# Performance work log

Measured on AMD Instinct MI355X. Metric: run time of the kernel, lower is better.

## Reference

```python
import jax, jax.numpy as jnp
import numpy as np

VOCAB = 32000
EMBED_DIM = 64
HIDDEN_NUM = 16
PAD_ID = 0
B, S = 128, 4096


def setup_inputs() -> dict:
    key = jax.random.key(0)
    k1, k2, k3, k4, k5, k6, k7 = jax.random.split(key, 7)
    # values serve as token ids (when mask==1) or numeric values (mask==0)
    input_ids = jax.random.randint(k1, (B, S), 0, VOCAB).astype(jnp.float32)
    type_mask = jax.random.randint(k2, (B, S), 0, 2).astype(jnp.int32)
    emb_table = jax.random.normal(k3, (VOCAB, EMBED_DIM), dtype=jnp.float32)
    emb_table = emb_table.at[PAD_ID].set(0.0)  # nn.Embedding padding_idx
    # numeric MLP: Linear(1,16) -> ReLU -> Linear(16,64)
    w1 = jax.random.normal(k4, (HIDDEN_NUM, 1), dtype=jnp.float32) * 0.5
    b1 = jax.random.normal(k5, (HIDDEN_NUM,), dtype=jnp.float32) * 0.1
    w2 = jax.random.normal(k6, (EMBED_DIM, HIDDEN_NUM), dtype=jnp.float32) * 0.25
    b2 = jax.random.normal(k7, (EMBED_DIM,), dtype=jnp.float32) * 0.1
    return {"input_ids": input_ids, "type_mask": type_mask,
            "emb_table": emb_table, "w1": w1, "b1": b1, "w2": w2, "b2": b2}


def reference(input_ids, type_mask, emb_table, w1, b1, w2, b2):
    # Faithful to Embedder.forward: token positions get embedding lookup,
    # numeric positions get a 2-layer MLP on the scalar value. Instead of
    # boolean gather/scatter (dynamic shapes), compute both paths densely
    # and select -- same math, jit-friendly, single pass.
    tok_mask = type_mask.astype(bool)                              # (B,S)
    ids = jnp.where(tok_mask, input_ids, 0).astype(jnp.int32)      # safe ids
    tok_emb = emb_table[ids]                                       # (B,S,D)
    x = input_ids[..., None]                                       # (B,S,1)
    h = jax.nn.relu(jnp.einsum('bsi,hi->bsh', x, w1) + b1)         # (B,S,16)
    num_emb = jnp.einsum('bsh,dh->bsd', h, w2) + b2                # (B,S,D)
    return jnp.where(tok_mask[..., None], tok_emb, num_emb)
```

## Files before the change

### kernel.cpp

```cpp
#include <hip/hip_runtime.h>

#define D 64
#define H 16

__global__ __launch_bounds__(256) void Embedder_kernel(
    const float* __restrict__ input_ids,
    const int*   __restrict__ type_mask,
    const float* __restrict__ emb,
    const float* __restrict__ w1,
    const float* __restrict__ b1,
    const float* __restrict__ w2,
    const float* __restrict__ b2,
    float*       __restrict__ out,
    int npos)
{
    __shared__ float s_w1[H];
    __shared__ float s_b1[H];
    __shared__ float s_b2[D];
    __shared__ float s_w2t[H * D];

    const int tid = threadIdx.x;
    if (tid < H) { s_w1[tid] = w1[tid]; s_b1[tid] = b1[tid]; }
    if (tid >= 64 && tid < 64 + D) s_b2[tid - 64] = b2[tid - 64];
    for (int i = tid; i < D * H; i += 256) {
        int d = i >> 4, j = i & 15;
        s_w2t[j * D + d] = w2[i];
    }
    __syncthreads();

    const int gid = blockIdx.x * 256 + tid;
    const int pos = gid >> 4;
    if (pos >= npos) return;
    const int d4 = (gid & 15) * 4;

    const float x = input_ids[pos];
    const int   m = type_mask[pos];

    float4 r;
    if (m) {
        const int id = (int)x;
        r = *reinterpret_cast<const float4*>(&emb[(size_t)id * D + d4]);
    } else {
        float h[H];
        #pragma unroll
        for (int j = 0; j < H; ++j)
            h[j] = fmaxf(fmaf(x, s_w1[j], s_b1[j]), 0.0f);
        float4 acc = *reinterpret_cast<const float4*>(&s_b2[d4]);
        #pragma unroll
        for (int j = 0; j < H; ++j) {
            const float4 w = *reinterpret_cast<const float4*>(&s_w2t[j * D + d4]);
            acc.x = fmaf(h[j], w.x, acc.x);
            acc.y = fmaf(h[j], w.y, acc.y);
            acc.z = fmaf(h[j], w.z, acc.z);
            acc.w = fmaf(h[j], w.w, acc.w);
        }
        r = acc;
    }
    *reinterpret_cast<float4*>(&out[(size_t)pos * D + d4]) = r;
}

extern "C" void kernel_launch(void* const* d_in, const int* in_sizes, int n_in,
                              void* d_out, int out_size, void* d_ws, size_t ws_size,
                              hipStream_t stream) {
    const float* input_ids = (const float*)d_in[0];
    const int*   type_mask = (const int*)d_in[1];
    const float* emb       = (const float*)d_in[2];
    const float* w1        = (const float*)d_in[3];
    const float* b1        = (const float*)d_in[4];
    const float* w2        = (const float*)d_in[5];
    const float* b2        = (const float*)d_in[6];
    float*       out       = (float*)d_out;

    const int npos = in_sizes[0];
    const long long nthreads = (long long)npos * 16;
    const int blocks = (int)((nthreads + 255) / 256);

    Embedder_kernel<<<blocks, 256, 0, stream>>>(
        input_ids, type_mask, emb, w1, b1, w2, b2, out, npos);
}
```

Baseline: 202.2 us.

## Process multiple positions per thread with register-resident MLP weights and branchless select

```diff
diff --git a/kernel.cpp b/kernel.cpp
--- a/kernel.cpp
+++ b/kernel.cpp
@@ -2,8 +2,11 @@
 
 #define D 64
 #define H 16
+#define PPT 16
 
-__global__ __launch_bounds__(256) void Embedder_kernel(
+typedef float f32x4 __attribute__((ext_vector_type(4)));
+
+__global__ __launch_bounds__(256, 3) void Embedder_kernel(
     const float* __restrict__ input_ids,
     const int*   __restrict__ type_mask,
     const float* __restrict__ emb,
@@ -14,49 +17,71 @@
     float*       __restrict__ out,
     int npos)
 {
-    __shared__ float s_w1[H];
-    __shared__ float s_b1[H];
-    __shared__ float s_b2[D];
-    __shared__ float s_w2t[H * D];
+    const int tid = threadIdx.x;
+    const int gid = blockIdx.x * 256 + tid;
+    const int T   = (npos * 16) / PPT;
+    if (gid >= T) return;
 
-    const int tid = threadIdx.x;
-    if (tid < H) { s_w1[tid] = w1[tid]; s_b1[tid] = b1[tid]; }
-    if (tid >= 64 && tid < 64 + D) s_b2[tid - 64] = b2[tid - 64];
-    for (int i = tid; i < D * H; i += 256) {
-        int d = i >> 4, j = i & 15;
-        s_w2t[j * D + d] = w2[i];
-    }
-    __syncthreads();
-
-    const int gid = blockIdx.x * 256 + tid;
-    const int pos = gid >> 4;
-    if (pos >= npos) return;
     const int d4 = (gid & 15) * 4;
 
-    const float x = input_ids[pos];
-    const int   m = type_mask[pos];
+    float w2s[4][H];
+    #pragma unroll
+    for (int r = 0; r < 4; ++r) {
+        #pragma unroll
+        for (int c = 0; c < 4; ++c) {
+            const f32x4 t = *reinterpret_cast<const f32x4*>(&w2[(d4 + r) * H + 4 * c]);
+            w2s[r][4*c+0] = t.x; w2s[r][4*c+1] = t.y;
+            w2s[r][4*c+2] = t.z; w2s[r][4*c+3] = t.w;
+        }
+    }
+    float w1r[H], b1r[H];
+    #pragma unroll
+    for (int c = 0; c < 4; ++c) {
+        const f32x4 tw = *reinterpret_cast<const f32x4*>(&w1[4*c]);
+        const f32x4 tb = *reinterpret_cast<const f32x4*>(&b1[4*c]);
+        w1r[4*c+0] = tw.x; w1r[4*c+1] = tw.y; w1r[4*c+2] = tw.z; w1r[4*c+3] = tw.w;
+        b1r[4*c+0] = tb.x; b1r[4*c+1] = tb.y; b1r[4*c+2] = tb.z; b1r[4*c+3] = tb.w;
+    }
+    const f32x4 b2s = *reinterpret_cast<const f32x4*>(&b2[d4]);
 
-    float4 r;
-    if (m) {
-        const int id = (int)x;
-        r = *reinterpret_cast<const float4*>(&emb[(size_t)id * D + d4]);
-    } else {
-        float h[H];
-        #pragma unroll
-        for (int j = 0; j < H; ++j)
-            h[j] = fmaxf(fmaf(x, s_w1[j], s_b1[j]), 0.0f);
-        float4 acc = *reinterpret_cast<const float4*>(&s_b2[d4]);
+    const int pbase = gid >> 4;
+    const int pstep = T >> 4;
+
+    #pragma unroll 1
+    for (int k = 0; k < PPT; k += 2) {
+        const int p0 = pbase + k * pstep;
+        const int p1 = p0 + pstep;
+
+        const float x0 = input_ids[p0];
+        const float x1 = input_ids[p1];
+        const int   m0 = type_mask[p0];
+        const int   m1 = type_mask[p1];
+
+        const int id0 = m0 ? (int)x0 : 0;
+        const int id1 = m1 ? (int)x1 : 0;
+        const f32x4 g0 = *reinterpret_cast<const f32x4*>(&emb[(size_t)id0 * D + d4]);
+        const f32x4 g1 = *reinterpret_cast<const f32x4*>(&emb[(size_t)id1 * D + d4]);
+
+        f32x4 a0 = b2s, a1 = b2s;
         #pragma unroll
         for (int j = 0; j < H; ++j) {
-            const float4 w = *reinterpret_cast<const float4*>(&s_w2t[j * D + d4]);
-            acc.x = fmaf(h[j], w.x, acc.x);
-            acc.y = fmaf(h[j], w.y, acc.y);
-            acc.z = fmaf(h[j], w.z, acc.z);
-            acc.w = fmaf(h[j], w.w, acc.w);
+            const float h0 = fmaxf(fmaf(x0, w1r[j], b1r[j]), 0.0f);
+            const float h1 = fmaxf(fmaf(x1, w1r[j], b1r[j]), 0.0f);
+            a0.x = fmaf(h0, w2s[0][j], a0.x);  a1.x = fmaf(h1, w2s[0][j], a1.x);
+            a0.y = fmaf(h0, w2s[1][j], a0.y);  a1.y = fmaf(h1, w2s[1][j], a1.y);
+            a0.z = fmaf(h0, w2s[2][j], a0.z);  a1.z = fmaf(h1, w2s[2][j], a1.z);
+            a0.w = fmaf(h0, w2s[3][j], a0.w);  a1.w = fmaf(h1, w2s[3][j], a1.w);
         }
-        r = acc;
+
+        f32x4 r0, r1;
+        r0.x = m0 ? g0.x : a0.x;  r0.y = m0 ? g0.y : a0.y;
+        r0.z = m0 ? g0.z : a0.z;  r0.w = m0 ? g0.w : a0.w;
+        r1.x = m1 ? g1.x : a1.x;  r1.y = m1 ? g1.y : a1.y;
+        r1.z = m1 ? g1.z : a1.z;  r1.w = m1 ? g1.w : a1.w;
+
+        __builtin_nontemporal_store(r0, reinterpret_cast<f32x4*>(&out[(size_t)p0 * D + d4]));
+        __builtin_nontemporal_store(r1, reinterpret_cast<f32x4*>(&out[(size_t)p1 * D + d4]));
     }
-    *reinterpret_cast<float4*>(&out[(size_t)pos * D + d4]) = r;
 }
 
 extern "C" void kernel_launch(void* const* d_in, const int* in_sizes, int n_in,
@@ -72,8 +97,8 @@
     float*       out       = (float*)d_out;
 
     const int npos = in_sizes[0];
-    const long long nthreads = (long long)npos * 16;
-    const int blocks = (int)((nthreads + 255) / 256);
+    const long long T = (long long)npos * 16 / PPT;
+    const int blocks = (int)((T + 255) / 256);
 
     Embedder_kernel<<<blocks, 256, 0, stream>>>(
         input_ids, type_mask, emb, w1, b1, w2, b2, out, npos);
```

Result: faster. 184.5 us (-8.8%).
